# Optimization experiments

Measured on AMD Instinct MI355X. Metric: run time of the kernel, lower is better.

Reference implementation:

```python
import jax, jax.numpy as jnp
import numpy as np

N = 50000
E = 800000
IN_C = 128
HID = 16
HEADS = 8
OUT_C = 128
NEG_SLOPE = 0.2
EPS = 1e-16


def setup_inputs() -> dict:
    key = jax.random.key(0)
    ks = jax.random.split(key, 12)
    x = jax.random.normal(ks[0], (N, IN_C), dtype=jnp.float32)
    edge_index = jax.random.randint(ks[1], (2, E), 0, N, dtype=jnp.int32)
    s1 = 1.0 / np.sqrt(IN_C)
    s2 = 1.0 / np.sqrt(HID * HEADS)
    W1 = jax.random.normal(ks[2], (IN_C, HEADS * HID), dtype=jnp.float32) * s1
    att_src1 = jax.random.normal(ks[3], (HEADS, HID), dtype=jnp.float32) * s1
    att_dst1 = jax.random.normal(ks[4], (HEADS, HID), dtype=jnp.float32) * s1
    b1 = jnp.zeros((HEADS * HID,), dtype=jnp.float32)
    W2 = jax.random.normal(ks[5], (HEADS * HID, OUT_C), dtype=jnp.float32) * s2
    att_src2 = jax.random.normal(ks[6], (1, OUT_C), dtype=jnp.float32) * s2
    att_dst2 = jax.random.normal(ks[7], (1, OUT_C), dtype=jnp.float32) * s2
    b2 = jnp.zeros((OUT_C,), dtype=jnp.float32)
    return {"x": x, "edge_index": edge_index, "W1": W1, "att_src1": att_src1,
            "att_dst1": att_dst1, "b1": b1, "W2": W2, "att_src2": att_src2,
            "att_dst2": att_dst2, "b2": b2}


def _add_self_loops(edge_index, n):
    loop = jnp.arange(n, dtype=edge_index.dtype)
    src = jnp.concatenate([edge_index[0], loop])
    dst = jnp.concatenate([edge_index[1], loop])
    return src, dst


def gat_conv(x, src, dst, W, att_src, att_dst, bias, heads, out_c, concat):
    n = x.shape[0]
    h = (x @ W).reshape(n, heads, out_c)          # [N, H, C]
    a_src = jnp.einsum('nhc,hc->nh', h, att_src)  # [N, H]
    a_dst = jnp.einsum('nhc,hc->nh', h, att_dst)
    e = a_src[src] + a_dst[dst]                   # [E', H]
    e = jax.nn.leaky_relu(e, NEG_SLOPE)
    # segment softmax over edges grouped by destination node
    m = jax.ops.segment_max(e, dst, num_segments=n)          # [N, H]
    m = jnp.where(jnp.isfinite(m), m, 0.0)
    ex = jnp.exp(e - m[dst])                                  # [E', H]
    denom = jax.ops.segment_sum(ex, dst, num_segments=n)      # [N, H]
    alpha = ex / (denom[dst] + EPS)                            # [E', H]
    msg = alpha[:, :, None] * h[src]                           # [E', H, C]
    out = jax.ops.segment_sum(msg, dst, num_segments=n)       # [N, H, C]
    if concat:
        out = out.reshape(n, heads * out_c)
    else:
        out = out.mean(axis=1)
    return out + bias


def reference(x, edge_index, W1, att_src1, att_dst1, b1, W2, att_src2, att_dst2, b2):
    src, dst = _add_self_loops(edge_index, N)
    h = gat_conv(x, src, dst, W1, att_src1, att_dst1, b1, HEADS, HID, True)
    h = jax.nn.relu(h)
    # dropout is identity in eval mode
    out = gat_conv(h, src, dst, W2, att_src2, att_dst2, b2, 1, OUT_C, False)
    return out
```

## Files before the change

kernel.cpp:

```cpp
#include <hip/hip_runtime.h>


constexpr int N_NODES = 50000;
constexpr int E_EDGES = 800000;
constexpr int ETOT = E_EDGES + N_NODES;
constexpr float NEG_SLOPE = 0.2f;
constexpr float EPS = 1e-16f;
constexpr int SCAN_BLK = 512;
constexpr int NBLK_SCAN = (N_NODES + SCAN_BLK - 1) / SCAN_BLK;

typedef short bf16x8 __attribute__((ext_vector_type(8)));
typedef float f32x4 __attribute__((ext_vector_type(4)));

__device__ __forceinline__ float lrelu(float x) { return x > 0.f ? x : NEG_SLOPE * x; }
__device__ __forceinline__ ushort f2bf(float f) {
    uint u = __float_as_uint(f);
    return (ushort)((u + 0x7fffu + ((u >> 16) & 1u)) >> 16);
}
__device__ __forceinline__ float bf2f(uint u) { return __uint_as_float(u << 16); }

__device__ __forceinline__ void fma8(float* acc, uint4 p, float w, float& ws) {
    ws += w;
    acc[0] += w * bf2f(p.x & 0xffffu); acc[1] += w * bf2f(p.x >> 16);
    acc[2] += w * bf2f(p.y & 0xffffu); acc[3] += w * bf2f(p.y >> 16);
    acc[4] += w * bf2f(p.z & 0xffffu); acc[5] += w * bf2f(p.z >> 16);
    acc[6] += w * bf2f(p.w & 0xffffu); acc[7] += w * bf2f(p.w >> 16);
}

__global__ __launch_bounds__(256) void convert_W(const float* __restrict__ W1,
                                                 const float* __restrict__ W2,
                                                 const float* __restrict__ attS2,
                                                 const float* __restrict__ attD2,
                                                 ushort* __restrict__ W1t,
                                                 ushort* __restrict__ W2t,
                                                 float* __restrict__ vs,
                                                 float* __restrict__ vd,
                                                 uint* __restrict__ cnt16) {
    const int t = threadIdx.x;
    if (blockIdx.x >= 2) {
        const int i = (blockIdx.x - 2) * 256 + t;
        if (i < (N_NODES + 1) / 2) cnt16[i] = 0;
        return;
    }
    const float* W = (blockIdx.x == 0) ? W1 : W2;
    ushort* Wt = (blockIdx.x == 0) ? W1t : W2t;
    const int n = t >> 1, k0 = (t & 1) * 64;
    for (int k = 0; k < 64; k += 2) {
        uint lo = f2bf(W[(size_t)(k0 + k) * 128 + n]);
        uint hi = f2bf(W[(size_t)(k0 + k + 1) * 128 + n]);
        *(uint*)&Wt[(size_t)n * 128 + k0 + k] = lo | (hi << 16);
    }
    if (blockIdx.x == 1) {
        const int k = t & 127;
        const float* av = (t < 128) ? attS2 : attD2;
        float* dst = (t < 128) ? vs : vd;
        float s = 0.f;
        for (int c = 0; c < 128; ++c) s += W2[(size_t)k * 128 + c] * av[c];
        dst[k] = s;
    }
}

__global__ __launch_bounds__(256) void count_rank(const int* __restrict__ ei,
                                                  uint* __restrict__ cnt16,
                                                  ushort* __restrict__ rank) {
    int e = blockIdx.x * blockDim.x + threadIdx.x;
    if (e >= ETOT) return;
    int d = (e < E_EDGES) ? ei[E_EDGES + e] : (e - E_EDGES);
    const uint shift = (d & 1) * 16;
    uint old = atomicAdd(&cnt16[d >> 1], 1u << shift);
    rank[e] = (ushort)((old >> shift) & 0xffffu);
}

__device__ __forceinline__ uint cnt_at(const uint* cnt16, int i) {
    return (cnt16[i >> 1] >> ((i & 1) * 16)) & 0xffffu;
}

__global__ __launch_bounds__(SCAN_BLK) void block_sums(const uint* __restrict__ cnt16,
                                                       int* __restrict__ bsum) {
    __shared__ int sm[SCAN_BLK];
    int i = blockIdx.x * SCAN_BLK + threadIdx.x;
    sm[threadIdx.x] = (i < N_NODES) ? (int)cnt_at(cnt16, i) : 0;
    __syncthreads();
    for (int off = SCAN_BLK / 2; off > 0; off >>= 1) {
        if (threadIdx.x < off) sm[threadIdx.x] += sm[threadIdx.x + off];
        __syncthreads();
    }
    if (threadIdx.x == 0) bsum[blockIdx.x] = sm[0];
}

__global__ __launch_bounds__(SCAN_BLK) void scan_final_fused(const uint* __restrict__ cnt16,
                                                             const int* __restrict__ bsum,
                                                             int* __restrict__ rowptr) {
    __shared__ int sb[128];
    __shared__ int sm[SCAN_BLK];
    const int t = threadIdx.x;
    if (t < 128) sb[t] = (t < NBLK_SCAN) ? bsum[t] : 0;
    __syncthreads();
    for (int off = 1; off < 128; off <<= 1) {
        int v = 0;
        if (t < 128 && t >= off) v = sb[t - off];
        __syncthreads();
        if (t < 128) sb[t] += v;
        __syncthreads();
    }
    const int bid = blockIdx.x;
    const int bpre = sb[bid] - bsum[bid];

    const int i = bid * SCAN_BLK + t;
    const int v = (i < N_NODES) ? (int)cnt_at(cnt16, i) : 0;
    sm[t] = v;
    __syncthreads();
    for (int off = 1; off < SCAN_BLK; off <<= 1) {
        int x = (t >= off) ? sm[t - off] : 0;
        __syncthreads();
        sm[t] += x;
        __syncthreads();
    }
    if (i < N_NODES) rowptr[i] = bpre + sm[t] - v;
    if (bid == 0 && t == 0) rowptr[N_NODES] = ETOT;
}

__global__ __launch_bounds__(256) void scatter_kernel(const int* __restrict__ ei,
                                                      const int* __restrict__ rowptr,
                                                      const ushort* __restrict__ rank,
                                                      int* __restrict__ csrc) {
    int e = blockIdx.x * blockDim.x + threadIdx.x;
    if (e >= ETOT) return;
    int s, d;
    if (e < E_EDGES) { s = ei[e]; d = ei[E_EDGES + e]; }
    else             { s = d = e - E_EDGES; }
    const int pos = rowptr[d] + (int)rank[e];
    __builtin_nontemporal_store(s, &csrc[pos]);
}

template <bool BF16IN, bool ATT8, bool ATTIN>
__global__ __launch_bounds__(256) void mfma_gemm(const void* __restrict__ Xv,
                                                 const ushort* __restrict__ Wt,
                                                 ushort* __restrict__ H,
                                                 const float* __restrict__ attS,
                                                 const float* __restrict__ attD,
                                                 float* __restrict__ aS,
                                                 float* __restrict__ aD,
                                                 int nrows) {
    __shared__ __align__(16) char smem[16384 + 32768];
    ushort* lx = (ushort*)smem;
    ushort* lw = (ushort*)(smem + 16384);
    float*  hs = (float*)smem;

    const int t = threadIdx.x;
    const int r0 = blockIdx.x * 64;

    {
        const int n = t >> 1, half = t & 1;
        const ushort* src = Wt + (size_t)n * 128 + half * 64;
        #pragma unroll
        for (int c = 0; c < 8; ++c) {
            int cx = half * 8 + c;
            uint4 v = *(const uint4*)(src + c * 8);
            *(uint4*)&lw[(n * 16 + (cx ^ (n & 7))) * 8] = v;
        }
    }
    {
        const int r = t >> 2, q = t & 3;
        const int grow = r0 + r;
        const uint4 z = {0, 0, 0, 0};
        #pragma unroll
        for (int cc = 0; cc < 4; ++cc) {
            int cx = q * 4 + cc;
            uint4 packed = z;
            if (grow < nrows) {
                if (BF16IN) {
                    packed = *(const uint4*)((const ushort*)Xv + (size_t)grow * 128 + cx * 8);
                } else {
                    const float* X = (const float*)Xv;
                    const float4 f0 = *(const float4*)(X + (size_t)grow * 128 + cx * 8);
                    const float4 f1 = *(const float4*)(X + (size_t)grow * 128 + cx * 8 + 4);
                    packed.x = (uint)f2bf(f0.x) | ((uint)f2bf(f0.y) << 16);
                    packed.y = (uint)f2bf(f0.z) | ((uint)f2bf(f0.w) << 16);
                    packed.z = (uint)f2bf(f1.x) | ((uint)f2bf(f1.y) << 16);
                    packed.w = (uint)f2bf(f1.z) | ((uint)f2bf(f1.w) << 16);
                }
            }
            *(uint4*)&lx[(r * 16 + (cx ^ (r & 7))) * 8] = packed;
        }
    }
    __syncthreads();

    const int wv = t >> 6, l = t & 63;
    const int row = wv * 16 + (l & 15);
    const int lg = l >> 4;
    f32x4 acc[8] = {};

    #pragma unroll
    for (int kb = 0; kb < 4; ++kb) {
        const int cx = kb * 4 + lg;
        bf16x8 a = *(const bf16x8*)&lx[(row * 16 + (cx ^ (row & 7))) * 8];
        #pragma unroll
        for (int nt = 0; nt < 8; ++nt) {
            const int n = nt * 16 + (l & 15);
            bf16x8 b = *(const bf16x8*)&lw[(n * 16 + (cx ^ (n & 7))) * 8];
            acc[nt] = __builtin_amdgcn_mfma_f32_16x16x32_bf16(a, b, acc[nt], 0, 0, 0);
        }
    }

    #pragma unroll
    for (int reg = 0; reg < 4; ++reg) {
        const int grow = r0 + wv * 16 + lg * 4 + reg;
        if (grow < nrows) {
            #pragma unroll
            for (int nt = 0; nt < 8; ++nt)
                H[(size_t)grow * 128 + nt * 16 + (l & 15)] = f2bf(acc[nt][reg]);
        }
    }

    if (ATT8) {
        __syncthreads();
        #pragma unroll
        for (int reg = 0; reg < 4; ++reg) {
            const int r = wv * 16 + lg * 4 + reg;
            #pragma unroll
            for (int nt = 0; nt < 8; ++nt)
                hs[r * 130 + nt * 16 + (l & 15)] = acc[nt][reg];
        }
        __syncthreads();
        for (int q = t; q < 512; q += 256) {
            const int r = q >> 3, h = q & 7;
            if (r0 + r < nrows) {
                float sv = 0.f, dv = 0.f;
                #pragma unroll
                for (int j = 0; j < 16; ++j) {
                    const float hv = hs[r * 130 + h * 16 + j];
                    sv += hv * attS[h * 16 + j];
                    dv += hv * attD[h * 16 + j];
                }
                aS[(size_t)(r0 + r) * 8 + h] = sv;
                aD[(size_t)(r0 + r) * 8 + h] = dv;
            }
        }
    }

    if (ATTIN) {
        const int r = t >> 2, qq = t & 3;
        float ps = 0.f, pd = 0.f;
        #pragma unroll
        for (int cc = 0; cc < 4; ++cc) {
            const int cx = qq * 4 + cc;
            const uint4 p = *(const uint4*)&lx[(r * 16 + (cx ^ (r & 7))) * 8];
            const uint w[4] = {p.x, p.y, p.z, p.w};
            #pragma unroll
            for (int q = 0; q < 4; ++q) {
                const float e0 = bf2f(w[q] & 0xffffu);
                const float e1 = bf2f(w[q] >> 16);
                ps += e0 * attS[cx * 8 + 2 * q] + e1 * attS[cx * 8 + 2 * q + 1];
                pd += e0 * attD[cx * 8 + 2 * q] + e1 * attD[cx * 8 + 2 * q + 1];
            }
        }
        ps += __shfl_xor(ps, 1); ps += __shfl_xor(ps, 2);
        pd += __shfl_xor(pd, 1); pd += __shfl_xor(pd, 2);
        if (qq == 0 && r0 + r < nrows) { aS[r0 + r] = ps; aD[r0 + r] = pd; }
    }
}

#define GISSUE(P, JJ)                                                          \
    {                                                                          \
        const int jx_ = (JJ);                                                  \
        const int sx_ = __shfl(s_l, jx_ & 63);                                 \
        P = zero4;                                                             \
        if (jx_ < rem) P = *(const uint4*)(Hm + (size_t)sx_ * 128 + i * 8);    \
    }

__global__ __launch_bounds__(256) void agg8(const int* __restrict__ rowptr,
                                            const int* __restrict__ csrc,
                                            const float* __restrict__ aS,
                                            const float* __restrict__ aD,
                                            const ushort* __restrict__ Hm,
                                            const float* __restrict__ bias,
                                            ushort* __restrict__ o1bf) {
    __shared__ float wlds[4][512];
    const int wv = threadIdx.x >> 6;
    const int d = blockIdx.x * 4 + wv;
    const int lane = threadIdx.x & 63;
    const int g = lane >> 4, i = lane & 15, hc = i >> 1;
    const int hw = lane & 7;
    const float adh = aD[(size_t)d * 8 + hw];

    const int base = rowptr[d], end = rowptr[d + 1];
    float acc[8] = {0.f, 0.f, 0.f, 0.f, 0.f, 0.f, 0.f, 0.f};
    float ws = 0.f;
    const uint4 zero4 = {0, 0, 0, 0};

    for (int c0 = base; c0 < end; c0 += 64) {
        const int rem = min(64, end - c0);
        const int s_l = (lane < rem) ? csrc[c0 + lane] : 0;

        uint4 ring[6];
        #pragma unroll
        for (int s = 0; s < 6; ++s) GISSUE(ring[s], 4 * s + g);

        const int nwc = (rem + 7) >> 3;
        for (int jj = 0; jj < nwc; ++jj) {
            const int j = jj * 8 + (lane >> 3);
            const int sj = __shfl(s_l, j & 63);
            float w = 0.f;
            if (j < rem) w = __expf(lrelu(aS[(size_t)sj * 8 + hw] + adh));
            wlds[wv][j * 8 + hw] = w;
        }

        const int niter = (rem + 3) >> 2;
        for (int tb = 0; tb < niter; tb += 6) {
            #pragma unroll
            for (int s = 0; s < 6; ++s) {
                if (tb + s < niter) {
                    const int j = (tb + s) * 4 + g;
                    const float w = (j < rem) ? wlds[wv][j * 8 + hc] : 0.f;
                    fma8(acc, ring[s], w, ws);
                    GISSUE(ring[s], j + 24);
                }
            }
        }
    }

    #pragma unroll
    for (int k = 0; k < 8; ++k) {
        acc[k] += __shfl_xor(acc[k], 16);
        acc[k] += __shfl_xor(acc[k], 32);
    }
    ws += __shfl_xor(ws, 16);
    ws += __shfl_xor(ws, 32);

    if (g == 0) {
        const float inv = 1.f / (ws + EPS);
        float v[8];
        #pragma unroll
        for (int k = 0; k < 8; ++k) v[k] = fmaxf(acc[k] * inv + bias[i * 8 + k], 0.f);
        uint4 pk;
        pk.x = (uint)f2bf(v[0]) | ((uint)f2bf(v[1]) << 16);
        pk.y = (uint)f2bf(v[2]) | ((uint)f2bf(v[3]) << 16);
        pk.z = (uint)f2bf(v[4]) | ((uint)f2bf(v[5]) << 16);
        pk.w = (uint)f2bf(v[6]) | ((uint)f2bf(v[7]) << 16);
        *(uint4*)(o1bf + (size_t)d * 128 + i * 8) = pk;
    }
}

__global__ __launch_bounds__(256) void agg1(const int* __restrict__ rowptr,
                                            const int* __restrict__ csrc,
                                            const float* __restrict__ aS,
                                            const float* __restrict__ aD,
                                            const ushort* __restrict__ Hm,
                                            const float* __restrict__ bias,
                                            float* __restrict__ out) {
    const int wv = threadIdx.x >> 6;
    const int d = blockIdx.x * 4 + wv;
    const int lane = threadIdx.x & 63;
    const int g = lane >> 4, i = lane & 15;
    const float ad = aD[d];

    const int base = rowptr[d], end = rowptr[d + 1];
    float acc[8] = {0.f, 0.f, 0.f, 0.f, 0.f, 0.f, 0.f, 0.f};
    float ws = 0.f;
    const uint4 zero4 = {0, 0, 0, 0};

    for (int c0 = base; c0 < end; c0 += 64) {
        const int rem = min(64, end - c0);
        const int s_l = (lane < rem) ? csrc[c0 + lane] : 0;

        uint4 ring[6];
        #pragma unroll
        for (int s = 0; s < 6; ++s) GISSUE(ring[s], 4 * s + g);

        const float w_l = (lane < rem) ? __expf(lrelu(aS[s_l] + ad)) : 0.f;

        const int niter = (rem + 3) >> 2;
        for (int tb = 0; tb < niter; tb += 6) {
            #pragma unroll
            for (int s = 0; s < 6; ++s) {
                if (tb + s < niter) {
                    const int j = (tb + s) * 4 + g;
                    const float wr = __shfl(w_l, j & 63);
                    const float w = (j < rem) ? wr : 0.f;
                    fma8(acc, ring[s], w, ws);
                    GISSUE(ring[s], j + 24);
                }
            }
        }
    }

    #pragma unroll
    for (int k = 0; k < 8; ++k) {
        acc[k] += __shfl_xor(acc[k], 16);
        acc[k] += __shfl_xor(acc[k], 32);
    }
    ws += __shfl_xor(ws, 16);
    ws += __shfl_xor(ws, 32);

    if (g == 0) {
        const float inv = 1.f / (ws + EPS);
        float4 o0, o1v;
        o0.x = acc[0] * inv + bias[i * 8 + 0];
        o0.y = acc[1] * inv + bias[i * 8 + 1];
        o0.z = acc[2] * inv + bias[i * 8 + 2];
        o0.w = acc[3] * inv + bias[i * 8 + 3];
        o1v.x = acc[4] * inv + bias[i * 8 + 4];
        o1v.y = acc[5] * inv + bias[i * 8 + 5];
        o1v.z = acc[6] * inv + bias[i * 8 + 6];
        o1v.w = acc[7] * inv + bias[i * 8 + 7];
        *(float4*)(out + (size_t)d * 128 + i * 8) = o0;
        *(float4*)(out + (size_t)d * 128 + i * 8 + 4) = o1v;
    }
}

extern "C" void kernel_launch(void* const* d_in, const int* in_sizes, int n_in,
                              void* d_out, int out_size, void* d_ws, size_t ws_size,
                              hipStream_t stream) {
    const float* x        = (const float*)d_in[0];
    const int*   ei       = (const int*)  d_in[1];
    const float* W1       = (const float*)d_in[2];
    const float* att_src1 = (const float*)d_in[3];
    const float* att_dst1 = (const float*)d_in[4];
    const float* b1       = (const float*)d_in[5];
    const float* W2       = (const float*)d_in[6];
    const float* att_src2 = (const float*)d_in[7];
    const float* att_dst2 = (const float*)d_in[8];
    const float* b2       = (const float*)d_in[9];
    float* out = (float*)d_out;

    ushort* Hbf  = (ushort*)d_ws;
    ushort* o1bf = Hbf + (size_t)N_NODES * 128;
    float*  aS1  = (float*)(o1bf + (size_t)N_NODES * 128);
    float*  aD1  = aS1 + (size_t)N_NODES * 8;
    float*  aS2  = aD1 + (size_t)N_NODES * 8;
    float*  aD2  = aS2 + N_NODES;
    float*  vs   = aD2 + N_NODES;
    float*  vd   = vs + 128;
    ushort* W1t  = (ushort*)(vd + 128);
    ushort* W2t  = W1t + 128 * 128;
    uint* cnt16  = (uint*)(W2t + 128 * 128);
    int* rowptr  = (int*)(cnt16 + (N_NODES + 1) / 2 + 1);
    int* bsum    = rowptr + N_NODES + 1;
    ushort* rank = (ushort*)(bsum + 128);
    int* csrc    = (int*)(rank + ETOT + 2);

    const int zblk = ((N_NODES + 1) / 2 + 255) / 256;
    const int eblk = (ETOT + 255) / 256;
    const int gemm_blocks = (N_NODES + 63) / 64;
    const int agg_blocks = N_NODES / 4;

    convert_W<<<2 + zblk, 256, 0, stream>>>(W1, W2, att_src2, att_dst2,
                                            W1t, W2t, vs, vd, cnt16);
    count_rank<<<eblk, 256, 0, stream>>>(ei, cnt16, rank);
    block_sums<<<NBLK_SCAN, SCAN_BLK, 0, stream>>>(cnt16, bsum);
    scan_final_fused<<<NBLK_SCAN, SCAN_BLK, 0, stream>>>(cnt16, bsum, rowptr);
    scatter_kernel<<<eblk, 256, 0, stream>>>(ei, rowptr, rank, csrc);

    mfma_gemm<false, true, false><<<gemm_blocks, 256, 0, stream>>>(
        x, W1t, Hbf, att_src1, att_dst1, aS1, aD1, N_NODES);
    agg8<<<agg_blocks, 256, 0, stream>>>(rowptr, csrc, aS1, aD1, Hbf, b1, o1bf);

    mfma_gemm<true, false, true><<<gemm_blocks, 256, 0, stream>>>(
        o1bf, W2t, Hbf, vs, vd, aS2, aD2, N_NODES);
    agg1<<<agg_blocks, 256, 0, stream>>>(rowptr, csrc, aS2, aD2, Hbf, b2, out);
}
```

Before: 211.2 us.

## Use full-width degree counters, 16-bit CSR indices, persistent aggregation waves with double buffering

Replaces the packed 16-bit degree counters with one 32-bit counter per node, so count_rank no longer needs shift-and-mask atomics. Stores CSR source indices as ushort to halve index traffic. Turns agg8 and agg1 into grid-stride loops over nodes with a fixed 2048-block grid, and swaps the six-deep gather ring for a simple one-ahead prefetch. The ushort indices only hold node ids up to 65535 (N is 50000), and the shallower prefetch may expose more gather latency.

```diff
diff --git a/kernel.cpp b/kernel.cpp
--- a/kernel.cpp
+++ b/kernel.cpp
@@ -35,11 +35,11 @@
                                                  ushort* __restrict__ W2t,
                                                  float* __restrict__ vs,
                                                  float* __restrict__ vd,
-                                                 uint* __restrict__ cnt16) {
+                                                 uint* __restrict__ cnt) {
     const int t = threadIdx.x;
     if (blockIdx.x >= 2) {
         const int i = (blockIdx.x - 2) * 256 + t;
-        if (i < (N_NODES + 1) / 2) cnt16[i] = 0;
+        if (i < N_NODES) cnt[i] = 0;
         return;
     }
     const float* W = (blockIdx.x == 0) ? W1 : W2;
@@ -61,25 +61,20 @@
 }
 
 __global__ __launch_bounds__(256) void count_rank(const int* __restrict__ ei,
-                                                  uint* __restrict__ cnt16,
+                                                  uint* __restrict__ cnt,
                                                   ushort* __restrict__ rank) {
     int e = blockIdx.x * blockDim.x + threadIdx.x;
     if (e >= ETOT) return;
     int d = (e < E_EDGES) ? ei[E_EDGES + e] : (e - E_EDGES);
-    const uint shift = (d & 1) * 16;
-    uint old = atomicAdd(&cnt16[d >> 1], 1u << shift);
-    rank[e] = (ushort)((old >> shift) & 0xffffu);
-}
-
-__device__ __forceinline__ uint cnt_at(const uint* cnt16, int i) {
-    return (cnt16[i >> 1] >> ((i & 1) * 16)) & 0xffffu;
-}
-
-__global__ __launch_bounds__(SCAN_BLK) void block_sums(const uint* __restrict__ cnt16,
+    uint old = atomicAdd(&cnt[d], 1u);
+    rank[e] = (ushort)old;
+}
+
+__global__ __launch_bounds__(SCAN_BLK) void block_sums(const uint* __restrict__ cnt,
                                                        int* __restrict__ bsum) {
     __shared__ int sm[SCAN_BLK];
     int i = blockIdx.x * SCAN_BLK + threadIdx.x;
-    sm[threadIdx.x] = (i < N_NODES) ? (int)cnt_at(cnt16, i) : 0;
+    sm[threadIdx.x] = (i < N_NODES) ? (int)cnt[i] : 0;
     __syncthreads();
     for (int off = SCAN_BLK / 2; off > 0; off >>= 1) {
         if (threadIdx.x < off) sm[threadIdx.x] += sm[threadIdx.x + off];
@@ -88,7 +83,7 @@
     if (threadIdx.x == 0) bsum[blockIdx.x] = sm[0];
 }
 
-__global__ __launch_bounds__(SCAN_BLK) void scan_final_fused(const uint* __restrict__ cnt16,
+__global__ __launch_bounds__(SCAN_BLK) void scan_final_fused(const uint* __restrict__ cnt,
                                                              const int* __restrict__ bsum,
                                                              int* __restrict__ rowptr) {
     __shared__ int sb[128];
@@ -107,7 +102,7 @@
     const int bpre = sb[bid] - bsum[bid];
 
     const int i = bid * SCAN_BLK + t;
-    const int v = (i < N_NODES) ? (int)cnt_at(cnt16, i) : 0;
+    const int v = (i < N_NODES) ? (int)cnt[i] : 0;
     sm[t] = v;
     __syncthreads();
     for (int off = 1; off < SCAN_BLK; off <<= 1) {
@@ -123,14 +118,14 @@
 __global__ __launch_bounds__(256) void scatter_kernel(const int* __restrict__ ei,
                                                       const int* __restrict__ rowptr,
                                                       const ushort* __restrict__ rank,
-                                                      int* __restrict__ csrc) {
+                                                      ushort* __restrict__ csrc) {
     int e = blockIdx.x * blockDim.x + threadIdx.x;
     if (e >= ETOT) return;
     int s, d;
     if (e < E_EDGES) { s = ei[e]; d = ei[E_EDGES + e]; }
     else             { s = d = e - E_EDGES; }
     const int pos = rowptr[d] + (int)rank[e];
-    __builtin_nontemporal_store(s, &csrc[pos]);
+    __builtin_nontemporal_store((ushort)s, &csrc[pos]);
 }
 
 template <bool BF16IN, bool ATT8, bool ATTIN>
@@ -261,16 +256,8 @@
     }
 }
 
-#define GISSUE(P, JJ)                                                          \
-    {                                                                          \
-        const int jx_ = (JJ);                                                  \
-        const int sx_ = __shfl(s_l, jx_ & 63);                                 \
-        P = zero4;                                                             \
-        if (jx_ < rem) P = *(const uint4*)(Hm + (size_t)sx_ * 128 + i * 8);    \
-    }
-
 __global__ __launch_bounds__(256) void agg8(const int* __restrict__ rowptr,
-                                            const int* __restrict__ csrc,
+                                            const ushort* __restrict__ csrc,
                                             const float* __restrict__ aS,
                                             const float* __restrict__ aD,
                                             const ushort* __restrict__ Hm,
@@ -278,134 +265,140 @@
                                             ushort* __restrict__ o1bf) {
     __shared__ float wlds[4][512];
     const int wv = threadIdx.x >> 6;
-    const int d = blockIdx.x * 4 + wv;
     const int lane = threadIdx.x & 63;
     const int g = lane >> 4, i = lane & 15, hc = i >> 1;
     const int hw = lane & 7;
-    const float adh = aD[(size_t)d * 8 + hw];
-
-    const int base = rowptr[d], end = rowptr[d + 1];
-    float acc[8] = {0.f, 0.f, 0.f, 0.f, 0.f, 0.f, 0.f, 0.f};
-    float ws = 0.f;
+    const int wid = blockIdx.x * 4 + wv;
+    const int nw = gridDim.x * 4;
     const uint4 zero4 = {0, 0, 0, 0};
 
-    for (int c0 = base; c0 < end; c0 += 64) {
-        const int rem = min(64, end - c0);
-        const int s_l = (lane < rem) ? csrc[c0 + lane] : 0;
-
-        uint4 ring[6];
-        #pragma unroll
-        for (int s = 0; s < 6; ++s) GISSUE(ring[s], 4 * s + g);
-
-        const int nwc = (rem + 7) >> 3;
-        for (int jj = 0; jj < nwc; ++jj) {
-            const int j = jj * 8 + (lane >> 3);
-            const int sj = __shfl(s_l, j & 63);
-            float w = 0.f;
-            if (j < rem) w = __expf(lrelu(aS[(size_t)sj * 8 + hw] + adh));
-            wlds[wv][j * 8 + hw] = w;
-        }
-
-        const int niter = (rem + 3) >> 2;
-        for (int tb = 0; tb < niter; tb += 6) {
+    for (int d = wid; d < N_NODES; d += nw) {
+        const float adh = aD[(size_t)d * 8 + hw];
+        const int base = rowptr[d], end = rowptr[d + 1];
+        float acc[8] = {0.f, 0.f, 0.f, 0.f, 0.f, 0.f, 0.f, 0.f};
+        float ws = 0.f;
+
+        for (int c0 = base; c0 < end; c0 += 64) {
+            const int rem = min(64, end - c0);
+            const int s_l = (lane < rem) ? (int)csrc[c0 + lane] : 0;
+
+            const int nwc = (rem + 7) >> 3;
+            for (int jj = 0; jj < nwc; ++jj) {
+                const int j = jj * 8 + (lane >> 3);
+                const int sj = __shfl(s_l, j & 63);
+                float w = 0.f;
+                if (j < rem) w = __expf(lrelu(aS[(size_t)sj * 8 + hw] + adh));
+                wlds[wv][j * 8 + hw] = w;
+            }
+
+            const int niter = (rem + 3) >> 2;
+            int j = g;
+            int scur = __shfl(s_l, j);
+            uint4 pcur = zero4;
+            if (j < rem) pcur = *(const uint4*)(Hm + (size_t)scur * 128 + i * 8);
+            for (int tt = 0; tt < niter; ++tt) {
+                const int jn = j + 4;
+                const int snxt = __shfl(s_l, jn & 63);
+                uint4 pnxt = zero4;
+                if (jn < rem) pnxt = *(const uint4*)(Hm + (size_t)snxt * 128 + i * 8);
+                float w = 0.f;
+                if (j < rem) w = wlds[wv][j * 8 + hc];
+                fma8(acc, pcur, w, ws);
+                pcur = pnxt;
+                j = jn;
+            }
+        }
+
+        #pragma unroll
+        for (int k = 0; k < 8; ++k) {
+            acc[k] += __shfl_xor(acc[k], 16);
+            acc[k] += __shfl_xor(acc[k], 32);
+        }
+        ws += __shfl_xor(ws, 16);
+        ws += __shfl_xor(ws, 32);
+
+        if (g == 0) {
+            const float inv = 1.f / (ws + EPS);
+            float v[8];
             #pragma unroll
-            for (int s = 0; s < 6; ++s) {
-                if (tb + s < niter) {
-                    const int j = (tb + s) * 4 + g;
-                    const float w = (j < rem) ? wlds[wv][j * 8 + hc] : 0.f;
-                    fma8(acc, ring[s], w, ws);
-                    GISSUE(ring[s], j + 24);
-                }
-            }
-        }
-    }
-
-    #pragma unroll
-    for (int k = 0; k < 8; ++k) {
-        acc[k] += __shfl_xor(acc[k], 16);
-        acc[k] += __shfl_xor(acc[k], 32);
-    }
-    ws += __shfl_xor(ws, 16);
-    ws += __shfl_xor(ws, 32);
-
-    if (g == 0) {
-        const float inv = 1.f / (ws + EPS);
-        float v[8];
-        #pragma unroll
-        for (int k = 0; k < 8; ++k) v[k] = fmaxf(acc[k] * inv + bias[i * 8 + k], 0.f);
-        uint4 pk;
-        pk.x = (uint)f2bf(v[0]) | ((uint)f2bf(v[1]) << 16);
-        pk.y = (uint)f2bf(v[2]) | ((uint)f2bf(v[3]) << 16);
-        pk.z = (uint)f2bf(v[4]) | ((uint)f2bf(v[5]) << 16);
-        pk.w = (uint)f2bf(v[6]) | ((uint)f2bf(v[7]) << 16);
-        *(uint4*)(o1bf + (size_t)d * 128 + i * 8) = pk;
+            for (int k = 0; k < 8; ++k) v[k] = fmaxf(acc[k] * inv + bias[i * 8 + k], 0.f);
+            uint4 pk;
+            pk.x = (uint)f2bf(v[0]) | ((uint)f2bf(v[1]) << 16);
+            pk.y = (uint)f2bf(v[2]) | ((uint)f2bf(v[3]) << 16);
+            pk.z = (uint)f2bf(v[4]) | ((uint)f2bf(v[5]) << 16);
+            pk.w = (uint)f2bf(v[6]) | ((uint)f2bf(v[7]) << 16);
+            *(uint4*)(o1bf + (size_t)d * 128 + i * 8) = pk;
+        }
     }
 }
 
 __global__ __launch_bounds__(256) void agg1(const int* __restrict__ rowptr,
-                                            const int* __restrict__ csrc,
+                                            const ushort* __restrict__ csrc,
                                             const float* __restrict__ aS,
                                             const float* __restrict__ aD,
                                             const ushort* __restrict__ Hm,
                                             const float* __restrict__ bias,
                                             float* __restrict__ out) {
     const int wv = threadIdx.x >> 6;
-    const int d = blockIdx.x * 4 + wv;
     const int lane = threadIdx.x & 63;
     const int g = lane >> 4, i = lane & 15;
-    const float ad = aD[d];
-
-    const int base = rowptr[d], end = rowptr[d + 1];
-    float acc[8] = {0.f, 0.f, 0.f, 0.f, 0.f, 0.f, 0.f, 0.f};
-    float ws = 0.f;
+    const int wid = blockIdx.x * 4 + wv;
+    const int nw = gridDim.x * 4;
     const uint4 zero4 = {0, 0, 0, 0};
 
-    for (int c0 = base; c0 < end; c0 += 64) {
-        const int rem = min(64, end - c0);
-        const int s_l = (lane < rem) ? csrc[c0 + lane] : 0;
-
-        uint4 ring[6];
-        #pragma unroll
-        for (int s = 0; s < 6; ++s) GISSUE(ring[s], 4 * s + g);
-
-        const float w_l = (lane < rem) ? __expf(lrelu(aS[s_l] + ad)) : 0.f;
-
-        const int niter = (rem + 3) >> 2;
-        for (int tb = 0; tb < niter; tb += 6) {
-            #pragma unroll
-            for (int s = 0; s < 6; ++s) {
-                if (tb + s < niter) {
-                    const int j = (tb + s) * 4 + g;
-                    const float wr = __shfl(w_l, j & 63);
-                    const float w = (j < rem) ? wr : 0.f;
-                    fma8(acc, ring[s], w, ws);
-                    GISSUE(ring[s], j + 24);
-                }
-            }
-        }
-    }
-
-    #pragma unroll
-    for (int k = 0; k < 8; ++k) {
-        acc[k] += __shfl_xor(acc[k], 16);
-        acc[k] += __shfl_xor(acc[k], 32);
-    }
-    ws += __shfl_xor(ws, 16);
-    ws += __shfl_xor(ws, 32);
-
-    if (g == 0) {
-        const float inv = 1.f / (ws + EPS);
-        float4 o0, o1v;
-        o0.x = acc[0] * inv + bias[i * 8 + 0];
-        o0.y = acc[1] * inv + bias[i * 8 + 1];
-        o0.z = acc[2] * inv + bias[i * 8 + 2];
-        o0.w = acc[3] * inv + bias[i * 8 + 3];
-        o1v.x = acc[4] * inv + bias[i * 8 + 4];
-        o1v.y = acc[5] * inv + bias[i * 8 + 5];
-        o1v.z = acc[6] * inv + bias[i * 8 + 6];
-        o1v.w = acc[7] * inv + bias[i * 8 + 7];
-        *(float4*)(out + (size_t)d * 128 + i * 8) = o0;
-        *(float4*)(out + (size_t)d * 128 + i * 8 + 4) = o1v;
+    for (int d = wid; d < N_NODES; d += nw) {
+        const float ad = aD[d];
+        const int base = rowptr[d], end = rowptr[d + 1];
+        float acc[8] = {0.f, 0.f, 0.f, 0.f, 0.f, 0.f, 0.f, 0.f};
+        float ws = 0.f;
+
+        for (int c0 = base; c0 < end; c0 += 64) {
+            const int rem = min(64, end - c0);
+            const int s_l = (lane < rem) ? (int)csrc[c0 + lane] : 0;
+            const float w_l = (lane < rem) ? __expf(lrelu(aS[s_l] + ad)) : 0.f;
+
+            const int niter = (rem + 3) >> 2;
+            int j = g;
+            int scur = __shfl(s_l, j);
+            float wcur = __shfl(w_l, j);
+            uint4 pcur = zero4;
+            if (j < rem) pcur = *(const uint4*)(Hm + (size_t)scur * 128 + i * 8);
+            for (int tt = 0; tt < niter; ++tt) {
+                const int jn = j + 4;
+                const int snxt = __shfl(s_l, jn & 63);
+                const float wnxt = __shfl(w_l, jn & 63);
+                uint4 pnxt = zero4;
+                if (jn < rem) pnxt = *(const uint4*)(Hm + (size_t)snxt * 128 + i * 8);
+                float w = (j < rem) ? wcur : 0.f;
+                fma8(acc, pcur, w, ws);
+                pcur = pnxt;
+                wcur = wnxt;
+                j = jn;
+            }
+        }
+
+        #pragma unroll
+        for (int k = 0; k < 8; ++k) {
+            acc[k] += __shfl_xor(acc[k], 16);
+            acc[k] += __shfl_xor(acc[k], 32);
+        }
+        ws += __shfl_xor(ws, 16);
+        ws += __shfl_xor(ws, 32);
+
+        if (g == 0) {
+            const float inv = 1.f / (ws + EPS);
+            float4 o0, o1v;
+            o0.x = acc[0] * inv + bias[i * 8 + 0];
+            o0.y = acc[1] * inv + bias[i * 8 + 1];
+            o0.z = acc[2] * inv + bias[i * 8 + 2];
+            o0.w = acc[3] * inv + bias[i * 8 + 3];
+            o1v.x = acc[4] * inv + bias[i * 8 + 4];
+            o1v.y = acc[5] * inv + bias[i * 8 + 5];
+            o1v.z = acc[6] * inv + bias[i * 8 + 6];
+            o1v.w = acc[7] * inv + bias[i * 8 + 7];
+            *(float4*)(out + (size_t)d * 128 + i * 8) = o0;
+            *(float4*)(out + (size_t)d * 128 + i * 8 + 4) = o1v;
+        }
     }
 }
 
@@ -434,22 +427,22 @@
     float*  vd   = vs + 128;
     ushort* W1t  = (ushort*)(vd + 128);
     ushort* W2t  = W1t + 128 * 128;
-    uint* cnt16  = (uint*)(W2t + 128 * 128);
-    int* rowptr  = (int*)(cnt16 + (N_NODES + 1) / 2 + 1);
+    uint* cnt    = (uint*)(W2t + 128 * 128);
+    int* rowptr  = (int*)(cnt + N_NODES + 1);
     int* bsum    = rowptr + N_NODES + 1;
     ushort* rank = (ushort*)(bsum + 128);
-    int* csrc    = (int*)(rank + ETOT + 2);
-
-    const int zblk = ((N_NODES + 1) / 2 + 255) / 256;
+    ushort* csrc = rank + ETOT + 2;
+
+    const int zblk = (N_NODES + 255) / 256;
     const int eblk = (ETOT + 255) / 256;
     const int gemm_blocks = (N_NODES + 63) / 64;
-    const int agg_blocks = N_NODES / 4;
+    const int agg_blocks = 2048;
 
     convert_W<<<2 + zblk, 256, 0, stream>>>(W1, W2, att_src2, att_dst2,
-                                            W1t, W2t, vs, vd, cnt16);
-    count_rank<<<eblk, 256, 0, stream>>>(ei, cnt16, rank);
-    block_sums<<<NBLK_SCAN, SCAN_BLK, 0, stream>>>(cnt16, bsum);
-    scan_final_fused<<<NBLK_SCAN, SCAN_BLK, 0, stream>>>(cnt16, bsum, rowptr);
+                                            W1t, W2t, vs, vd, cnt);
+    count_rank<<<eblk, 256, 0, stream>>>(ei, cnt, rank);
+    block_sums<<<NBLK_SCAN, SCAN_BLK, 0, stream>>>(cnt, bsum);
+    scan_final_fused<<<NBLK_SCAN, SCAN_BLK, 0, stream>>>(cnt, bsum, rowptr);
     scatter_kernel<<<eblk, 256, 0, stream>>>(ei, rowptr, rank, csrc);
 
     mfma_gemm<false, true, false><<<gemm_blocks, 256, 0, stream>>>(
```

New measurement: 198.8 us, median of 2. -5.8%, faster.
